# Kernel optimization log

Hardware: AMD Instinct MI355X
Metric: run time of the kernel (lower is better)

## Reference

```python
import math
import jax, jax.numpy as jnp
import numpy as np

HOP = 256
N_FFT = 1024
SR = 24000
B = 8
T = 1200          # feature frames
L = T * HOP       # 307200 audio samples
K_REV = 8192
BINS = N_FFT // 2 + 1


def setup_inputs() -> dict:
    key = jax.random.key(0)
    k1, k2, k3, k4, k5 = jax.random.split(key, 5)
    # realistic voiced f0 in [50, 400] Hz (forward gates on f0 > 20 Hz)
    f0 = 50.0 + 350.0 * jax.random.uniform(k1, (B, T), dtype=jnp.float32)
    env_per = jax.random.uniform(k2, (B, BINS, T), dtype=jnp.float32)
    env_noi = 0.1 * jax.random.uniform(k3, (B, BINS, T), dtype=jnp.float32)
    rev = 0.01 * jax.random.normal(k4, (B, K_REV), dtype=jnp.float32)
    # stands in for torch.rand_like(imp) inside forward (uniform [0,1))
    noi = jax.random.uniform(k5, (B, L), dtype=jnp.float32)
    # periodic Hann window, as torch.hann_window(n_fft)
    window = (0.5 - 0.5 * jnp.cos(2.0 * jnp.pi * jnp.arange(N_FFT) / N_FFT)).astype(jnp.float32)
    return {"f0": f0, "env_per": env_per, "env_noi": env_noi, "rev": rev, "noi": noi, "window": window}


def _interp_linear(x, scale):
    # torch F.interpolate(mode='linear', align_corners=False)
    Lx = x.shape[-1]
    out_len = Lx * scale
    src = (jnp.arange(out_len, dtype=jnp.float32) + 0.5) / scale - 0.5
    src = jnp.clip(src, 0.0, Lx - 1)
    i0 = jnp.floor(src).astype(jnp.int32)
    i1 = jnp.minimum(i0 + 1, Lx - 1)
    w = src - i0.astype(jnp.float32)
    return x[:, i0] * (1.0 - w) + x[:, i1] * w


def _stft(x, window):
    # torch.stft(center=True, pad_mode='reflect', return_complex=True)
    pad = N_FFT // 2
    xp = jnp.pad(x, ((0, 0), (pad, pad)), mode='reflect')
    n_frames = 1 + (xp.shape[-1] - N_FFT) // HOP
    idx = jnp.arange(n_frames)[:, None] * HOP + jnp.arange(N_FFT)[None, :]
    frames = xp[:, idx] * window                      # [B, F, N_FFT]
    return jnp.fft.rfft(frames, axis=-1).transpose(0, 2, 1)  # [B, BINS, F]


def _istft(spec, window):
    # torch.istft(center=True): windowed overlap-add with window-square normalization
    frames = jnp.fft.irfft(spec.transpose(0, 2, 1), n=N_FFT, axis=-1) * window  # [B, F, N_FFT]
    Bc, Fr, _ = frames.shape
    out_len = N_FFT + HOP * (Fr - 1)
    idx = (jnp.arange(Fr)[:, None] * HOP + jnp.arange(N_FFT)[None, :]).reshape(-1)
    out = jnp.zeros((Bc, out_len), frames.dtype).at[:, idx].add(frames.reshape(Bc, -1))
    wsq = jnp.zeros((out_len,), frames.dtype).at[idx].add(jnp.tile(window ** 2, Fr))
    out = out / jnp.where(wsq > 1e-11, wsq, 1.0)
    pad = N_FFT // 2
    return out[:, pad:out_len - pad]


def _min_phase(amp, eps=1e-5):
    # homomorphic minimum-phase reconstruction from real amplitude envelope
    # amp: [B, BINS, F]  ->  complex spectrum exp(rfft(lifted real cepstrum))
    log_amp = jnp.log(jnp.maximum(amp, eps))
    cep = jnp.fft.irfft(log_amp, n=N_FFT, axis=1)     # [B, N_FFT, F] real cepstrum
    lift = jnp.concatenate([
        jnp.ones((1,), jnp.float32),
        2.0 * jnp.ones((N_FFT // 2 - 1,), jnp.float32),
        jnp.ones((1,), jnp.float32),
        jnp.zeros((N_FFT // 2 - 1,), jnp.float32),
    ])
    return jnp.exp(jnp.fft.rfft(cep * lift[None, :, None], axis=1))  # [B, BINS, F]


def _fft_convolve(signal, kernel):
    # DDSP-style FFT convolution: zero-pad signal right, kernel left, multiply spectra
    Ls = signal.shape[-1]
    sig = jnp.pad(signal, ((0, 0), (0, Ls)))
    ker = jnp.pad(kernel, ((0, 0), (2 * Ls - kernel.shape[-1], 0)))
    out = jnp.fft.irfft(jnp.fft.rfft(sig) * jnp.fft.rfft(ker), n=2 * Ls)
    return out[:, Ls:]


def reference(f0, env_per, env_noi, rev, noi, window):
    env_per = jnp.pad(env_per, ((0, 0), (0, 0), (1, 0)))   # [B, BINS, T+1]
    env_noi = jnp.pad(env_noi, ((0, 0), (0, 0), (1, 0)))
    # sample-rate f0 track and impulse amplitude scale
    f0_up = _interp_linear(f0, HOP)                        # [B, L]
    imp_scale = jax.lax.rsqrt(jnp.maximum(f0_up, 20.0)) * math.sqrt(SR)
    # impulse train: fire where the running phase wraps past an integer
    phase = jnp.cumsum(f0_up, axis=-1) / SR
    saw = jnp.mod(phase, 1.0)
    imp = (saw - jnp.roll(saw, 1, axis=-1) < 0.0).astype(jnp.float32)
    imp = imp.at[:, 0].set(0.0)
    imp = imp * imp_scale
    imp_stft = _stft(imp, window)                          # [B, BINS, T+1]
    noi_stft = _stft(noi, window)
    # voiced/unvoiced gating of the periodic envelope
    mask = (jnp.pad(f0, ((0, 0), (1, 0)))[:, None, :] > 20.0).astype(jnp.float32)
    env_per = env_per * mask
    voi_stft = imp_stft * _min_phase(env_per) + noi_stft * env_noi
    voi = _istft(voi_stft, window)                         # [B, L]
    voi = _fft_convolve(voi, rev)                          # [B, L]
    return voi
```

## Files before the change

### kernel.cpp

```cpp
#include <hip/hip_runtime.h>
#include <math.h>

#define BB 8
#define TT 1200
#define NFFT 1024
#define BINS 513
#define LTOT 307200
#define KREV 8192
#define NFRM 34
#define NSAMP 8960
#define OUTOFF 299008
#define SQRT_SR 154.91933384829668f

#define OFF_FR   0

__device__ __forceinline__ int rev4_10(int n) {
    int r = (int)(__brev((unsigned)n) >> 22);
    return ((r & 0x155) << 1) | ((r & 0x2AA) >> 1);
}

__device__ __forceinline__ void dif4(float* re, float* im,
                                     const float* twr, const float* twi,
                                     float dir, int u, bool act) {
#pragma unroll
    for (int s = 0; s < 5; ++s) {
        const int q = 256 >> (2 * s);
        const int sh = 8 - 2 * s;
        __syncthreads();
        if (act) {
            int t = u & (q - 1);
            int base = ((u >> sh) << (sh + 2)) | t;
            int i0 = base, i1 = base + q, i2 = base + 2 * q, i3 = base + 3 * q;
            float ar = re[i0], ai = im[i0];
            float br = re[i1], bi = im[i1];
            float cr = re[i2], ci = im[i2];
            float dr = re[i3], di = im[i3];
            float t0r = ar + cr, t0i = ai + ci;
            float t1r = ar - cr, t1i = ai - ci;
            float t2r = br + dr, t2i = bi + di;
            float t3r = br - dr, t3i = bi - di;
            float y0r = t0r + t2r, y0i = t0i + t2i;
            float y2r = t0r - t2r, y2i = t0i - t2i;
            float y1r = t1r - dir * t3i, y1i = t1i + dir * t3r;
            float y3r = t1r + dir * t3i, y3i = t1i - dir * t3r;
            float c1 = twr[2 * q - 1 + t], s1 = twi[2 * q - 1 + t];
            float c2 = twr[q - 1 + t],     s2 = twi[q - 1 + t];
            float w1r = c1, w1i = dir * s1;
            float w2r = c2, w2i = dir * s2;
            float w3r = c1 * c2 - s1 * s2;
            float w3i = dir * (c1 * s2 + s1 * c2);
            re[i0] = y0r;                       im[i0] = y0i;
            re[i1] = y1r * w1r - y1i * w1i;     im[i1] = y1r * w1i + y1i * w1r;
            re[i2] = y2r * w2r - y2i * w2i;     im[i2] = y2r * w2i + y2i * w2r;
            re[i3] = y3r * w3r - y3i * w3i;     im[i3] = y3r * w3i + y3i * w3r;
        }
    }
    __syncthreads();
}

__device__ __forceinline__ void dit4(float* re, float* im,
                                     const float* twr, const float* twi,
                                     float dir, int u, bool act) {
#pragma unroll
    for (int s = 0; s < 5; ++s) {
        const int q = 1 << (2 * s);
        const int sh = 2 * s;
        __syncthreads();
        if (act) {
            int t = u & (q - 1);
            int base = ((u >> sh) << (sh + 2)) | t;
            int i0 = base, i1 = base + q, i2 = base + 2 * q, i3 = base + 3 * q;
            float c1 = twr[2 * q - 1 + t], s1 = twi[2 * q - 1 + t];
            float c2 = twr[q - 1 + t],     s2 = twi[q - 1 + t];
            float w1r = c1, w1i = dir * s1;
            float w2r = c2, w2i = dir * s2;
            float w3r = c1 * c2 - s1 * s2;
            float w3i = dir * (c1 * s2 + s1 * c2);
            float ar = re[i0], ai = im[i0];
            float xr = re[i1], xi = im[i1];
            float yr = re[i2], yi = im[i2];
            float zr = re[i3], zi = im[i3];
            float br = xr * w1r - xi * w1i, bi = xr * w1i + xi * w1r;
            float cr = yr * w2r - yi * w2i, ci = yr * w2i + yi * w2r;
            float dr = zr * w3r - zi * w3i, di = zr * w3i + zi * w3r;
            float t0r = ar + cr, t0i = ai + ci;
            float t1r = ar - cr, t1i = ai - ci;
            float t2r = br + dr, t2i = bi + di;
            float t3r = br - dr, t3i = bi - di;
            re[i0] = t0r + t2r;            im[i0] = t0i + t2i;
            re[i2] = t0r - t2r;            im[i2] = t0i - t2i;
            re[i1] = t1r - dir * t3i;      im[i1] = t1i + dir * t3r;
            re[i3] = t1r + dir * t3i;      im[i3] = t1i - dir * t3r;
        }
    }
    __syncthreads();
}

#define LV1 0
#define LV2 4480
#define LV3 6720
#define LV4 7840
#define LV5 8400
#define LV6 8680
#define LV7 8820
#define LV8 8890
#define LV9 8925
#define LV10 8942
#define LV11 8950
#define LV12 8954
#define LV13 8956

__global__ __launch_bounds__(512) void kfrm(const float* __restrict__ f0,
                                            const float* __restrict__ env_per,
                                            const float* __restrict__ env_noi,
                                            const float* __restrict__ noi,
                                            const float* __restrict__ win,
                                            float* __restrict__ W,
                                            float* __restrict__ out) {
    const int bid = blockIdx.x;
    const int tid = threadIdx.x;
    const int b = bid / 17;
    const int fp = (bid - b * 17) * 2;
    const int fg = fp + 1;

    __shared__ __align__(16) float SMEM[17917];
    __shared__ float cw[1281], fw[1281];
    __shared__ float twr[1023], twi[1023];

    {
        float4* out4 = (float4*)out;
        int g = bid * 512 + tid;
        for (int idx = g; idx < (BB * LTOT) / 4; idx += 136 * 512)
            out4[idx] = make_float4(0.f, 0.f, 0.f, 0.f);
    }
    for (int x = tid; x < 1023; x += 512) {
        int hb = 31 - __clz(x + 1);
        int half = 1 << hb;
        int t = (x + 1) - half;
        float a = 3.14159265358979323846f * ((float)t / (float)half);
        float sv, cv; sincosf(a, &sv, &cv);
        twr[x] = cv; twi[x] = sv;
    }

    float* F = SMEM;
    float* L = SMEM + 8960;
    for (int i = tid; i < NSAMP; i += 512) {
        float src = __fsub_rn(__fdiv_rn(__fadd_rn((float)i, 0.5f), 256.0f), 0.5f);
        src = fminf(fmaxf(src, 0.0f), (float)(TT - 1));
        int i0 = (int)floorf(src);
        int i1 = i0 + 1; if (i1 > TT - 1) i1 = TT - 1;
        float w = __fsub_rn(src, (float)i0);
        float a0 = __fmul_rn(f0[b * TT + i0], __fsub_rn(1.0f, w));
        float a1 = __fmul_rn(f0[b * TT + i1], w);
        F[i] = __fadd_rn(a0, a1);
    }
    __syncthreads();
    for (int j = tid; j < 2240; j += 512) {
        float a = __fadd_rn(F[4*j],     F[4*j + 1]);
        float c = __fadd_rn(F[4*j + 2], F[4*j + 3]);
        L[LV1 + 2*j] = a; L[LV1 + 2*j + 1] = c;
        L[LV2 + j] = __fadd_rn(a, c);
    }
    __syncthreads();
    for (int j = tid; j < 560; j += 512) {
        float a = __fadd_rn(L[LV2 + 4*j],     L[LV2 + 4*j + 1]);
        float c = __fadd_rn(L[LV2 + 4*j + 2], L[LV2 + 4*j + 3]);
        L[LV3 + 2*j] = a; L[LV3 + 2*j + 1] = c;
        L[LV4 + j] = __fadd_rn(a, c);
    }
    __syncthreads();
    if (tid < 140) {
        int j = tid;
        float a = __fadd_rn(L[LV4 + 4*j],     L[LV4 + 4*j + 1]);
        float c = __fadd_rn(L[LV4 + 4*j + 2], L[LV4 + 4*j + 3]);
        L[LV5 + 2*j] = a; L[LV5 + 2*j + 1] = c;
        L[LV6 + j] = __fadd_rn(a, c);
    }
    __syncthreads();
    if (tid < 35) {
        int j = tid;
        float a = __fadd_rn(L[LV6 + 4*j],     L[LV6 + 4*j + 1]);
        float c = __fadd_rn(L[LV6 + 4*j + 2], L[LV6 + 4*j + 3]);
        L[LV7 + 2*j] = a; L[LV7 + 2*j + 1] = c;
        L[LV8 + j] = __fadd_rn(a, c);
    }
    __syncthreads();
    if (tid < 9) {
        int j = tid;
        if (j < 8) {
            float a = __fadd_rn(L[LV8 + 4*j],     L[LV8 + 4*j + 1]);
            float c = __fadd_rn(L[LV8 + 4*j + 2], L[LV8 + 4*j + 3]);
            L[LV9 + 2*j] = a; L[LV9 + 2*j + 1] = c;
            L[LV10 + j] = __fadd_rn(a, c);
        } else {
            L[LV9 + 16] = __fadd_rn(L[LV8 + 32], L[LV8 + 33]);
        }
    }
    __syncthreads();
    if (tid == 0) {
        float a0 = __fadd_rn(L[LV10 + 0], L[LV10 + 1]);
        float a1 = __fadd_rn(L[LV10 + 2], L[LV10 + 3]);
        float a2 = __fadd_rn(L[LV10 + 4], L[LV10 + 5]);
        float a3 = __fadd_rn(L[LV10 + 6], L[LV10 + 7]);
        L[LV11 + 0] = a0; L[LV11 + 1] = a1; L[LV11 + 2] = a2; L[LV11 + 3] = a3;
        float b0 = __fadd_rn(a0, a1), b1 = __fadd_rn(a2, a3);
        L[LV12 + 0] = b0; L[LV12 + 1] = b1;
        L[LV13 + 0] = __fadd_rn(b0, b1);
    }
    __syncthreads();
    const int cbase = (fp >= 3) ? (256 * fp - 513) : 0;
    {
        const int offs[14] = {0, LV1, LV2, LV3, LV4, LV5, LV6, LV7, LV8, LV9, LV10, LV11, LV12, LV13};
        for (int w = tid; w < 1281; w += 512) {
            int p = cbase + w;
            if (p < NSAMP) {
                int n = p + 1;
                float acc = 0.f; int pos = 0; bool first = true;
#pragma unroll
                for (int k = 13; k >= 1; --k) {
                    if ((n >> k) & 1) {
                        float t = L[offs[k] + (pos >> k)];
                        acc = first ? t : __fadd_rn(acc, t);
                        first = false;
                        pos += (1 << k);
                    }
                }
                if (n & 1) {
                    float t = F[pos];
                    acc = first ? t : __fadd_rn(acc, t);
                }
                cw[w] = acc;
                fw[w] = F[p];
            }
        }
    }
    __syncthreads();

    float* wr_  = SMEM;
    float* wi_  = SMEM + 1024;
    float* zfr  = SMEM + 2048;
    float* zfi  = SMEM + 3072;
    float* zgr  = SMEM + 4096;
    float* zgi  = SMEM + 5120;
    float* mpfr = SMEM + 6144;
    float* mpfi = SMEM + 6660;
    float* mpgr = SMEM + 7176;
    float* mpgi = SMEM + 7692;
    const int u = tid & 255;
    const bool lo = (tid < 256);

    for (int k = tid; k < BINS; k += 512) {
        float epf = 0.0f;
        if (fp > 0) {
            float f0v = f0[b * TT + (fp - 1)];
            epf = (f0v > 20.0f) ? env_per[(size_t)(b * BINS + k) * TT + (fp - 1)] : 0.0f;
        }
        float f0g = f0[b * TT + (fg - 1)];
        float epg = (f0g > 20.0f) ? env_per[(size_t)(b * BINS + k) * TT + (fg - 1)] : 0.0f;
        mpfr[k] = logf(fmaxf(epf, 1e-5f));
        mpgr[k] = logf(fmaxf(epg, 1e-5f));
    }
    __syncthreads();
#pragma unroll
    for (int r = 0; r < 2; ++r) {
        int n = tid + 512 * r;
        int kv = (n <= 512) ? n : 1024 - n;
        wr_[n] = mpfr[kv];
        wi_[n] = mpgr[kv];
    }
    dif4(wr_, wi_, twr, twi, -1.f, u, lo);
    const float inv = 1.0f / 1024.0f;
#pragma unroll
    for (int r = 0; r < 2; ++r) {
        int p = tid + 512 * r;
        int n = rev4_10(p);
        float wgt = (n == 0 || n == 512) ? inv : ((n < 512) ? 2.0f * inv : 0.0f);
        wr_[p] *= wgt;
        wi_[p] *= wgt;
    }
    dit4(wr_, wi_, twr, twi, -1.f, u, lo);
    for (int k = tid; k < BINS; k += 512) {
        int mk = (1024 - k) & 1023;
        float yr = wr_[k], yi = wi_[k];
        float ymr = wr_[mk], ymi = -wi_[mk];
        float Lfr = 0.5f * (yr + ymr), Lfi = 0.5f * (yi + ymi);
        float dr = yr - ymr, di = yi - ymi;
        float Lgr = 0.5f * di, Lgi = -0.5f * dr;
        float ef = expf(Lfr);
        mpfr[k] = ef * cosf(Lfi); mpfi[k] = ef * sinf(Lfi);
        float eg = expf(Lgr);
        mpgr[k] = eg * cosf(Lgi); mpgi[k] = eg * sinf(Lgi);
    }
    __syncthreads();
#pragma unroll
    for (int r = 0; r < 2; ++r) {
        int n = tid + 512 * r;
        int i = 256 * fp + n - 512; if (i < 0) i = -i;
        float v = 0.0f;
        if (i > 0) {
            int iw = i - cbase;
            float ph  = __fdiv_rn(cw[iw], 24000.0f);
            float sw  = __fsub_rn(ph, floorf(ph));
            float ph2 = __fdiv_rn(cw[iw - 1], 24000.0f);
            float sw2 = __fsub_rn(ph2, floorf(ph2));
            if (__fsub_rn(sw, sw2) < 0.0f)
                v = __fmul_rn(__fdiv_rn(1.0f, __fsqrt_rn(fmaxf(fw[iw], 20.0f))), SQRT_SR);
        }
        float wv = win[n];
        zfr[n] = __fmul_rn(noi[b * LTOT + i], wv);
        zfi[n] = __fmul_rn(v, wv);
        int i2 = 256 * fg + n - 512; if (i2 < 0) i2 = -i2;
        float v2 = 0.0f;
        if (i2 > 0) {
            int iw = i2 - cbase;
            float ph  = __fdiv_rn(cw[iw], 24000.0f);
            float sw  = __fsub_rn(ph, floorf(ph));
            float ph2 = __fdiv_rn(cw[iw - 1], 24000.0f);
            float sw2 = __fsub_rn(ph2, floorf(ph2));
            if (__fsub_rn(sw, sw2) < 0.0f)
                v2 = __fmul_rn(__fdiv_rn(1.0f, __fsqrt_rn(fmaxf(fw[iw], 20.0f))), SQRT_SR);
        }
        zgr[n] = __fmul_rn(noi[b * LTOT + i2], wv);
        zgi[n] = __fmul_rn(v2, wv);
    }
    dif4(lo ? zfr : zgr, lo ? zfi : zgi, twr, twi, -1.f, u, true);
#pragma unroll
    for (int r = 0; r < 2; ++r) {
        int p = tid + 512 * r;
        int k = rev4_10(p);
        int kk = (k <= 512) ? k : 1024 - k;
        bool cj = (k > 512);
        int p1 = rev4_10(kk);
        int p2 = rev4_10((1024 - kk) & 1023);
        float vr, vi;
        {
            float z1r = zfr[p1], z1i = zfi[p1];
            float z2r = zfr[p2], z2i = -zfi[p2];
            float Nr = 0.5f * (z1r + z2r), Ni = 0.5f * (z1i + z2i);
            float dr = z1r - z2r, di = z1i - z2i;
            float Ir = 0.5f * di, Ii = -0.5f * dr;
            float mpr = mpfr[kk], mpi2 = mpfi[kk];
            float en = (fp == 0) ? 0.f : env_noi[(size_t)(b * BINS + kk) * TT + (fp - 1)];
            vr = Ir * mpr - Ii * mpi2 + Nr * en;
            vi = Ir * mpi2 + Ii * mpr + Ni * en;
            if (cj) vi = -vi;
        }
        float vgr, vgi;
        {
            float z1r = zgr[p1], z1i = zgi[p1];
            float z2r = zgr[p2], z2i = -zgi[p2];
            float Nr = 0.5f * (z1r + z2r), Ni = 0.5f * (z1i + z2i);
            float dr = z1r - z2r, di = z1i - z2i;
            float Ir = 0.5f * di, Ii = -0.5f * dr;
            float mpr = mpgr[kk], mpi2 = mpgi[kk];
            float en = env_noi[(size_t)(b * BINS + kk) * TT + (fg - 1)];
            vgr = Ir * mpr - Ii * mpi2 + Nr * en;
            vgi = Ir * mpi2 + Ii * mpr + Ni * en;
            if (cj) vgi = -vgi;
        }
        wr_[p] = vr - vgi;
        wi_[p] = vi + vgr;
    }
    dit4(wr_, wi_, twr, twi, +1.f, u, lo);
#pragma unroll
    for (int r = 0; r < 2; ++r) {
        int n = tid + 512 * r;
        float wv = win[n];
        W[OFF_FR + (((size_t)(b * NFRM + fp)) << 10) + n] = __fmul_rn(__fmul_rn(wr_[n], inv), wv);
        W[OFF_FR + (((size_t)(b * NFRM + fg)) << 10) + n] = __fmul_rn(__fmul_rn(wi_[n], inv), wv);
    }
}

__global__ __launch_bounds__(256) void k4(const float* __restrict__ rev,
                                          const float* __restrict__ win,
                                          const float* __restrict__ W,
                                          float* __restrict__ out) {
    const int tid = threadIdx.x;
    const int b = blockIdx.x / 72;
    int r = blockIdx.x - b * 72;
    int jt = 0, acc0 = 0;
    while (acc0 + 2 * (jt + 1) <= r) { acc0 += 2 * (jt + 1); ++jt; }
    const int mc = r - acc0;
    const int j0 = jt << 10, m0 = mc << 9;

    __shared__ __align__(16) float S[1536];
    const int base = j0 - m0 - 512;
    for (int x = tid; x < 1536; x += 256) {
        int j = base + x;
        float v = 0.f;
        if (j >= 0 && j < KREV) {
            int s = j + 512;
            int flo = (s >= 1023) ? ((s - 1023 + 255) >> 8) : 0;
            int fhi = s >> 8; if (fhi > NFRM - 1) fhi = NFRM - 1;
            float acc = 0.f, wsq = 0.f;
            for (int f = flo; f <= fhi; ++f) {
                int o = s - (f << 8);
                acc = __fadd_rn(acc, W[OFF_FR + (((size_t)(b * NFRM + f)) << 10) + o]);
                float wv = win[o];
                wsq = __fadd_rn(wsq, __fmul_rn(wv, wv));
            }
            float den = (wsq > 1e-11f) ? wsq : 1.0f;
            v = __fdiv_rn(acc, den);
        }
        S[x] = v;
    }
    __syncthreads();

    const float4* S4 = (const float4*)S;
    const float* Rb = rev + b * KREV + m0;
    float y0 = 0.f, y1 = 0.f, y2 = 0.f, y3 = 0.f;
    const int qi = tid + 128;
    float4 Bv = S4[qi];
#pragma unroll 4
    for (int mq = 0; mq < 128; ++mq) {
        float4 A = S4[qi - 1 - mq];
        float4 r4 = *(const float4*)(Rb + 4 * mq);
        y0 = fmaf(r4.x, Bv.x, y0); y0 = fmaf(r4.y, A.w,  y0); y0 = fmaf(r4.z, A.z,  y0); y0 = fmaf(r4.w, A.y,  y0);
        y1 = fmaf(r4.x, Bv.y, y1); y1 = fmaf(r4.y, Bv.x, y1); y1 = fmaf(r4.z, A.w,  y1); y1 = fmaf(r4.w, A.z,  y1);
        y2 = fmaf(r4.x, Bv.z, y2); y2 = fmaf(r4.y, Bv.y, y2); y2 = fmaf(r4.z, Bv.x, y2); y2 = fmaf(r4.w, A.w,  y2);
        y3 = fmaf(r4.x, Bv.w, y3); y3 = fmaf(r4.y, Bv.z, y3); y3 = fmaf(r4.z, Bv.y, y3); y3 = fmaf(r4.w, Bv.x, y3);
        Bv = A;
    }
    float* o = out + (size_t)b * LTOT + OUTOFF + j0 + 4 * tid;
    atomicAdd(o + 0, y0);
    atomicAdd(o + 1, y1);
    atomicAdd(o + 2, y2);
    atomicAdd(o + 3, y3);
}

extern "C" void kernel_launch(void* const* d_in, const int* in_sizes, int n_in,
                              void* d_out, int out_size, void* d_ws, size_t ws_size,
                              hipStream_t stream) {
    const float* f0      = (const float*)d_in[0];
    const float* env_per = (const float*)d_in[1];
    const float* env_noi = (const float*)d_in[2];
    const float* rev     = (const float*)d_in[3];
    const float* noi     = (const float*)d_in[4];
    const float* win     = (const float*)d_in[5];
    float* out = (float*)d_out;
    float* W   = (float*)d_ws;

    kfrm<<<dim3(136), dim3(512), 0, stream>>>(f0, env_per, env_noi, noi, win, W, out);
    k4<<<dim3(576),   dim3(256), 0, stream>>>(rev, win, W, out);
}
```

Baseline: 142.3 us.

## Swizzle FFT LDS indices, drop wave-local barriers, prefetch inputs, stage rev in LDS

Applies an XOR swizzle to every shared-memory FFT buffer index to spread accesses across LDS banks. In the radix-4 FFT stages whose butterflies stay inside one wavefront, the block-wide __syncthreads is replaced by an LDS wait. The per-frame global loads (env_per, env_noi, f0, noise samples and window) are issued at kernel start so their latency overlaps the twiddle setup and output zeroing. The convolution kernel copies its reverb slice into shared memory instead of reading it from global memory in the inner loop. The trade-offs are extra index arithmetic, more live registers for the prefetched values, and a correctness dependence on which stages are truly confined to one wavefront.

```diff
diff --git a/kernel.cpp b/kernel.cpp
--- a/kernel.cpp
+++ b/kernel.cpp
@@ -14,6 +14,8 @@
 
 #define OFF_FR   0
 
+#define PHI(i) ((i) ^ ((i) >> 5))
+
 __device__ __forceinline__ int rev4_10(int n) {
     int r = (int)(__brev((unsigned)n) >> 22);
     return ((r & 0x155) << 1) | ((r & 0x2AA) >> 1);
@@ -26,11 +28,12 @@
     for (int s = 0; s < 5; ++s) {
         const int q = 256 >> (2 * s);
         const int sh = 8 - 2 * s;
-        __syncthreads();
+        if (s < 2) __syncthreads();
+        else       asm volatile("s_waitcnt lgkmcnt(0)" ::: "memory");
         if (act) {
             int t = u & (q - 1);
             int base = ((u >> sh) << (sh + 2)) | t;
-            int i0 = base, i1 = base + q, i2 = base + 2 * q, i3 = base + 3 * q;
+            int i0 = PHI(base), i1 = PHI(base + q), i2 = PHI(base + 2 * q), i3 = PHI(base + 3 * q);
             float ar = re[i0], ai = im[i0];
             float br = re[i1], bi = im[i1];
             float cr = re[i2], ci = im[i2];
@@ -65,11 +68,12 @@
     for (int s = 0; s < 5; ++s) {
         const int q = 1 << (2 * s);
         const int sh = 2 * s;
-        __syncthreads();
+        if (s == 0 || s == 4) __syncthreads();
+        else                  asm volatile("s_waitcnt lgkmcnt(0)" ::: "memory");
         if (act) {
             int t = u & (q - 1);
             int base = ((u >> sh) << (sh + 2)) | t;
-            int i0 = base, i1 = base + q, i2 = base + 2 * q, i3 = base + 3 * q;
+            int i0 = PHI(base), i1 = PHI(base + q), i2 = PHI(base + 2 * q), i3 = PHI(base + 3 * q);
             float c1 = twr[2 * q - 1 + t], s1 = twi[2 * q - 1 + t];
             float c2 = twr[q - 1 + t],     s2 = twi[q - 1 + t];
             float w1r = c1, w1i = dir * s1;
@@ -127,6 +131,38 @@
     __shared__ float cw[1281], fw[1281];
     __shared__ float twr[1023], twi[1023];
 
+    const int idxF = (fp > 0) ? (fp - 1) : 0;
+    const int idxG = fg - 1;
+    float pfEpF = 0.f, pfEpG = 0.f, pfEpF2 = 0.f, pfEpG2 = 0.f;
+    {
+        pfEpF = env_per[((size_t)(b * BINS + tid)) * TT + idxF];
+        pfEpG = env_per[((size_t)(b * BINS + tid)) * TT + idxG];
+        if (tid == 0) {
+            pfEpF2 = env_per[((size_t)(b * BINS + 512)) * TT + idxF];
+            pfEpG2 = env_per[((size_t)(b * BINS + 512)) * TT + idxG];
+        }
+    }
+    const float pfF0F = f0[b * TT + idxF];
+    const float pfF0G = f0[b * TT + idxG];
+    int ktmp0 = rev4_10(tid);
+    const int kk0 = (ktmp0 <= 512) ? ktmp0 : 1024 - ktmp0;
+    int ktmp1 = rev4_10(tid + 512);
+    const int kk1 = (ktmp1 <= 512) ? ktmp1 : 1024 - ktmp1;
+    const float pfEnF0 = env_noi[((size_t)(b * BINS + kk0)) * TT + idxF];
+    const float pfEnG0 = env_noi[((size_t)(b * BINS + kk0)) * TT + idxG];
+    const float pfEnF1 = env_noi[((size_t)(b * BINS + kk1)) * TT + idxF];
+    const float pfEnG1 = env_noi[((size_t)(b * BINS + kk1)) * TT + idxG];
+    int iF0 = 256 * fp + tid - 512; if (iF0 < 0) iF0 = -iF0;
+    const int iF1 = 256 * fp + tid;
+    int iG0 = 256 * fg + tid - 512; if (iG0 < 0) iG0 = -iG0;
+    const int iG1 = 256 * fg + tid;
+    const float pfNoiF0 = noi[(size_t)b * LTOT + iF0];
+    const float pfNoiF1 = noi[(size_t)b * LTOT + iF1];
+    const float pfNoiG0 = noi[(size_t)b * LTOT + iG0];
+    const float pfNoiG1 = noi[(size_t)b * LTOT + iG1];
+    const float pfWin0 = win[tid];
+    const float pfWin1 = win[tid + 512];
+
     {
         float4* out4 = (float4*)out;
         int g = bid * 512 + tid;
@@ -249,24 +285,23 @@
     const int u = tid & 255;
     const bool lo = (tid < 256);
 
-    for (int k = tid; k < BINS; k += 512) {
-        float epf = 0.0f;
-        if (fp > 0) {
-            float f0v = f0[b * TT + (fp - 1)];
-            epf = (f0v > 20.0f) ? env_per[(size_t)(b * BINS + k) * TT + (fp - 1)] : 0.0f;
-        }
-        float f0g = f0[b * TT + (fg - 1)];
-        float epg = (f0g > 20.0f) ? env_per[(size_t)(b * BINS + k) * TT + (fg - 1)] : 0.0f;
-        mpfr[k] = logf(fmaxf(epf, 1e-5f));
-        mpgr[k] = logf(fmaxf(epg, 1e-5f));
+    {
+        const bool gF = (fp > 0) && (pfF0F > 20.0f);
+        const bool gG = (pfF0G > 20.0f);
+        mpfr[tid] = logf(fmaxf(gF ? pfEpF : 0.0f, 1e-5f));
+        mpgr[tid] = logf(fmaxf(gG ? pfEpG : 0.0f, 1e-5f));
+        if (tid == 0) {
+            mpfr[512] = logf(fmaxf(gF ? pfEpF2 : 0.0f, 1e-5f));
+            mpgr[512] = logf(fmaxf(gG ? pfEpG2 : 0.0f, 1e-5f));
+        }
     }
     __syncthreads();
 #pragma unroll
     for (int r = 0; r < 2; ++r) {
         int n = tid + 512 * r;
         int kv = (n <= 512) ? n : 1024 - n;
-        wr_[n] = mpfr[kv];
-        wi_[n] = mpgr[kv];
+        wr_[PHI(n)] = mpfr[kv];
+        wi_[PHI(n)] = mpgr[kv];
     }
     dif4(wr_, wi_, twr, twi, -1.f, u, lo);
     const float inv = 1.0f / 1024.0f;
@@ -275,14 +310,14 @@
         int p = tid + 512 * r;
         int n = rev4_10(p);
         float wgt = (n == 0 || n == 512) ? inv : ((n < 512) ? 2.0f * inv : 0.0f);
-        wr_[p] *= wgt;
-        wi_[p] *= wgt;
+        wr_[PHI(p)] *= wgt;
+        wi_[PHI(p)] *= wgt;
     }
     dit4(wr_, wi_, twr, twi, -1.f, u, lo);
     for (int k = tid; k < BINS; k += 512) {
         int mk = (1024 - k) & 1023;
-        float yr = wr_[k], yi = wi_[k];
-        float ymr = wr_[mk], ymi = -wi_[mk];
+        float yr = wr_[PHI(k)], yi = wi_[PHI(k)];
+        float ymr = wr_[PHI(mk)], ymi = -wi_[PHI(mk)];
         float Lfr = 0.5f * (yr + ymr), Lfi = 0.5f * (yi + ymi);
         float dr = yr - ymr, di = yi - ymi;
         float Lgr = 0.5f * di, Lgi = -0.5f * dr;
@@ -292,82 +327,109 @@
         mpgr[k] = eg * cosf(Lgi); mpgi[k] = eg * sinf(Lgi);
     }
     __syncthreads();
-#pragma unroll
-    for (int r = 0; r < 2; ++r) {
-        int n = tid + 512 * r;
-        int i = 256 * fp + n - 512; if (i < 0) i = -i;
-        float v = 0.0f;
-        if (i > 0) {
-            int iw = i - cbase;
-            float ph  = __fdiv_rn(cw[iw], 24000.0f);
-            float sw  = __fsub_rn(ph, floorf(ph));
-            float ph2 = __fdiv_rn(cw[iw - 1], 24000.0f);
-            float sw2 = __fsub_rn(ph2, floorf(ph2));
-            if (__fsub_rn(sw, sw2) < 0.0f)
-                v = __fmul_rn(__fdiv_rn(1.0f, __fsqrt_rn(fmaxf(fw[iw], 20.0f))), SQRT_SR);
-        }
-        float wv = win[n];
-        zfr[n] = __fmul_rn(noi[b * LTOT + i], wv);
-        zfi[n] = __fmul_rn(v, wv);
-        int i2 = 256 * fg + n - 512; if (i2 < 0) i2 = -i2;
-        float v2 = 0.0f;
-        if (i2 > 0) {
-            int iw = i2 - cbase;
-            float ph  = __fdiv_rn(cw[iw], 24000.0f);
-            float sw  = __fsub_rn(ph, floorf(ph));
-            float ph2 = __fdiv_rn(cw[iw - 1], 24000.0f);
-            float sw2 = __fsub_rn(ph2, floorf(ph2));
-            if (__fsub_rn(sw, sw2) < 0.0f)
-                v2 = __fmul_rn(__fdiv_rn(1.0f, __fsqrt_rn(fmaxf(fw[iw], 20.0f))), SQRT_SR);
-        }
-        zgr[n] = __fmul_rn(noi[b * LTOT + i2], wv);
-        zgi[n] = __fmul_rn(v2, wv);
+    {
+        {
+            const int n = tid;
+            float v = 0.0f;
+            int i = iF0;
+            if (i > 0) {
+                int iw = i - cbase;
+                float ph  = __fdiv_rn(cw[iw], 24000.0f);
+                float sw  = __fsub_rn(ph, floorf(ph));
+                float ph2 = __fdiv_rn(cw[iw - 1], 24000.0f);
+                float sw2 = __fsub_rn(ph2, floorf(ph2));
+                if (__fsub_rn(sw, sw2) < 0.0f)
+                    v = __fmul_rn(__fdiv_rn(1.0f, __fsqrt_rn(fmaxf(fw[iw], 20.0f))), SQRT_SR);
+            }
+            zfr[PHI(n)] = __fmul_rn(pfNoiF0, pfWin0);
+            zfi[PHI(n)] = __fmul_rn(v, pfWin0);
+            float v2 = 0.0f;
+            int i2 = iG0;
+            if (i2 > 0) {
+                int iw = i2 - cbase;
+                float ph  = __fdiv_rn(cw[iw], 24000.0f);
+                float sw  = __fsub_rn(ph, floorf(ph));
+                float ph2 = __fdiv_rn(cw[iw - 1], 24000.0f);
+                float sw2 = __fsub_rn(ph2, floorf(ph2));
+                if (__fsub_rn(sw, sw2) < 0.0f)
+                    v2 = __fmul_rn(__fdiv_rn(1.0f, __fsqrt_rn(fmaxf(fw[iw], 20.0f))), SQRT_SR);
+            }
+            zgr[PHI(n)] = __fmul_rn(pfNoiG0, pfWin0);
+            zgi[PHI(n)] = __fmul_rn(v2, pfWin0);
+        }
+        {
+            const int n = tid + 512;
+            float v = 0.0f;
+            int i = iF1;
+            if (i > 0) {
+                int iw = i - cbase;
+                float ph  = __fdiv_rn(cw[iw], 24000.0f);
+                float sw  = __fsub_rn(ph, floorf(ph));
+                float ph2 = __fdiv_rn(cw[iw - 1], 24000.0f);
+                float sw2 = __fsub_rn(ph2, floorf(ph2));
+                if (__fsub_rn(sw, sw2) < 0.0f)
+                    v = __fmul_rn(__fdiv_rn(1.0f, __fsqrt_rn(fmaxf(fw[iw], 20.0f))), SQRT_SR);
+            }
+            zfr[PHI(n)] = __fmul_rn(pfNoiF1, pfWin1);
+            zfi[PHI(n)] = __fmul_rn(v, pfWin1);
+            float v2 = 0.0f;
+            int i2 = iG1;
+            if (i2 > 0) {
+                int iw = i2 - cbase;
+                float ph  = __fdiv_rn(cw[iw], 24000.0f);
+                float sw  = __fsub_rn(ph, floorf(ph));
+                float ph2 = __fdiv_rn(cw[iw - 1], 24000.0f);
+                float sw2 = __fsub_rn(ph2, floorf(ph2));
+                if (__fsub_rn(sw, sw2) < 0.0f)
+                    v2 = __fmul_rn(__fdiv_rn(1.0f, __fsqrt_rn(fmaxf(fw[iw], 20.0f))), SQRT_SR);
+            }
+            zgr[PHI(n)] = __fmul_rn(pfNoiG1, pfWin1);
+            zgi[PHI(n)] = __fmul_rn(v2, pfWin1);
+        }
     }
     dif4(lo ? zfr : zgr, lo ? zfi : zgi, twr, twi, -1.f, u, true);
-#pragma unroll
-    for (int r = 0; r < 2; ++r) {
-        int p = tid + 512 * r;
-        int k = rev4_10(p);
-        int kk = (k <= 512) ? k : 1024 - k;
-        bool cj = (k > 512);
-        int p1 = rev4_10(kk);
-        int p2 = rev4_10((1024 - kk) & 1023);
-        float vr, vi;
-        {
-            float z1r = zfr[p1], z1i = zfi[p1];
-            float z2r = zfr[p2], z2i = -zfi[p2];
-            float Nr = 0.5f * (z1r + z2r), Ni = 0.5f * (z1i + z2i);
-            float dr = z1r - z2r, di = z1i - z2i;
-            float Ir = 0.5f * di, Ii = -0.5f * dr;
-            float mpr = mpfr[kk], mpi2 = mpfi[kk];
-            float en = (fp == 0) ? 0.f : env_noi[(size_t)(b * BINS + kk) * TT + (fp - 1)];
-            vr = Ir * mpr - Ii * mpi2 + Nr * en;
-            vi = Ir * mpi2 + Ii * mpr + Ni * en;
-            if (cj) vi = -vi;
-        }
-        float vgr, vgi;
-        {
-            float z1r = zgr[p1], z1i = zgi[p1];
-            float z2r = zgr[p2], z2i = -zgi[p2];
-            float Nr = 0.5f * (z1r + z2r), Ni = 0.5f * (z1i + z2i);
-            float dr = z1r - z2r, di = z1i - z2i;
-            float Ir = 0.5f * di, Ii = -0.5f * dr;
-            float mpr = mpgr[kk], mpi2 = mpgi[kk];
-            float en = env_noi[(size_t)(b * BINS + kk) * TT + (fg - 1)];
-            vgr = Ir * mpr - Ii * mpi2 + Nr * en;
-            vgi = Ir * mpi2 + Ii * mpr + Ni * en;
-            if (cj) vgi = -vgi;
-        }
-        wr_[p] = vr - vgi;
-        wi_[p] = vi + vgr;
+    {
+        auto vbuild = [&](int p, int kk, float enF, float enG) {
+            int k = rev4_10(p);
+            bool cj = (k > 512);
+            int p1 = rev4_10(kk);
+            int p2 = rev4_10((1024 - kk) & 1023);
+            float vr, vi;
+            {
+                float z1r = zfr[PHI(p1)], z1i = zfi[PHI(p1)];
+                float z2r = zfr[PHI(p2)], z2i = -zfi[PHI(p2)];
+                float Nr = 0.5f * (z1r + z2r), Ni = 0.5f * (z1i + z2i);
+                float dr = z1r - z2r, di = z1i - z2i;
+                float Ir = 0.5f * di, Ii = -0.5f * dr;
+                float mpr = mpfr[kk], mpi2 = mpfi[kk];
+                vr = Ir * mpr - Ii * mpi2 + Nr * enF;
+                vi = Ir * mpi2 + Ii * mpr + Ni * enF;
+                if (cj) vi = -vi;
+            }
+            float vgr, vgi;
+            {
+                float z1r = zgr[PHI(p1)], z1i = zgi[PHI(p1)];
+                float z2r = zgr[PHI(p2)], z2i = -zgi[PHI(p2)];
+                float Nr = 0.5f * (z1r + z2r), Ni = 0.5f * (z1i + z2i);
+                float dr = z1r - z2r, di = z1i - z2i;
+                float Ir = 0.5f * di, Ii = -0.5f * dr;
+                float mpr = mpgr[kk], mpi2 = mpgi[kk];
+                vgr = Ir * mpr - Ii * mpi2 + Nr * enG;
+                vgi = Ir * mpi2 + Ii * mpr + Ni * enG;
+                if (cj) vgi = -vgi;
+            }
+            wr_[PHI(p)] = vr - vgi;
+            wi_[PHI(p)] = vi + vgr;
+        };
+        vbuild(tid,       kk0, (fp == 0) ? 0.0f : pfEnF0, pfEnG0);
+        vbuild(tid + 512, kk1, (fp == 0) ? 0.0f : pfEnF1, pfEnG1);
     }
     dit4(wr_, wi_, twr, twi, +1.f, u, lo);
-#pragma unroll
-    for (int r = 0; r < 2; ++r) {
-        int n = tid + 512 * r;
-        float wv = win[n];
-        W[OFF_FR + (((size_t)(b * NFRM + fp)) << 10) + n] = __fmul_rn(__fmul_rn(wr_[n], inv), wv);
-        W[OFF_FR + (((size_t)(b * NFRM + fg)) << 10) + n] = __fmul_rn(__fmul_rn(wi_[n], inv), wv);
+    {
+        W[OFF_FR + (((size_t)(b * NFRM + fp)) << 10) + tid]       = __fmul_rn(__fmul_rn(wr_[PHI(tid)], inv), pfWin0);
+        W[OFF_FR + (((size_t)(b * NFRM + fg)) << 10) + tid]       = __fmul_rn(__fmul_rn(wi_[PHI(tid)], inv), pfWin0);
+        W[OFF_FR + (((size_t)(b * NFRM + fp)) << 10) + tid + 512] = __fmul_rn(__fmul_rn(wr_[PHI(tid + 512)], inv), pfWin1);
+        W[OFF_FR + (((size_t)(b * NFRM + fg)) << 10) + tid + 512] = __fmul_rn(__fmul_rn(wi_[PHI(tid + 512)], inv), pfWin1);
     }
 }
 
@@ -384,6 +446,9 @@
     const int j0 = jt << 10, m0 = mc << 9;
 
     __shared__ __align__(16) float S[1536];
+    __shared__ __align__(16) float Rv[512];
+    for (int x = tid; x < 512; x += 256)
+        Rv[x] = rev[b * KREV + m0 + x];
     const int base = j0 - m0 - 512;
     for (int x = tid; x < 1536; x += 256) {
         int j = base + x;
@@ -407,14 +472,14 @@
     __syncthreads();
 
     const float4* S4 = (const float4*)S;
-    const float* Rb = rev + b * KREV + m0;
+    const float4* R4 = (const float4*)Rv;
     float y0 = 0.f, y1 = 0.f, y2 = 0.f, y3 = 0.f;
     const int qi = tid + 128;
     float4 Bv = S4[qi];
 #pragma unroll 4
     for (int mq = 0; mq < 128; ++mq) {
         float4 A = S4[qi - 1 - mq];
-        float4 r4 = *(const float4*)(Rb + 4 * mq);
+        float4 r4 = R4[mq];
         y0 = fmaf(r4.x, Bv.x, y0); y0 = fmaf(r4.y, A.w,  y0); y0 = fmaf(r4.z, A.z,  y0); y0 = fmaf(r4.w, A.y,  y0);
         y1 = fmaf(r4.x, Bv.y, y1); y1 = fmaf(r4.y, Bv.x, y1); y1 = fmaf(r4.z, A.w,  y1); y1 = fmaf(r4.w, A.z,  y1);
         y2 = fmaf(r4.x, Bv.z, y2); y2 = fmaf(r4.y, Bv.y, y2); y2 = fmaf(r4.z, Bv.x, y2); y2 = fmaf(r4.w, A.w,  y2);
```

Measured after the change: 142.1 us. No clear change (-0.1%).
